# Optimization experiments

Hardware: AMD Instinct MI355X
Metric: run time of the kernel (lower is better)

Reference implementation:

```python
import jax, jax.numpy as jnp
import numpy as np

NUM_ITEMS = 50000
IN_FEATS = 64
H_FEATS = 64
NUM_EDGES = 800000


def setup_inputs() -> dict:
    key = jax.random.key(0)
    ks = jax.random.split(key, 12)
    s_in = 1.0 / np.sqrt(IN_FEATS)
    s_h = 1.0 / np.sqrt(H_FEATS)
    return {
        "embed": jax.random.normal(ks[0], (NUM_ITEMS, IN_FEATS), jnp.float32),
        "W1_self": jax.random.normal(ks[1], (IN_FEATS, H_FEATS), jnp.float32) * s_in,
        "W1_neigh": jax.random.normal(ks[2], (IN_FEATS, H_FEATS), jnp.float32) * s_in,
        "b1": jax.random.normal(ks[3], (H_FEATS,), jnp.float32) * s_in,
        "W2_self": jax.random.normal(ks[4], (H_FEATS, H_FEATS), jnp.float32) * s_h,
        "W2_neigh": jax.random.normal(ks[5], (H_FEATS, H_FEATS), jnp.float32) * s_h,
        "b2": jax.random.normal(ks[6], (H_FEATS,), jnp.float32) * s_h,
        "W_fc": jax.random.normal(ks[7], (H_FEATS, IN_FEATS), jnp.float32) * s_h,
        "b_fc": jax.random.normal(ks[8], (IN_FEATS,), jnp.float32) * s_h,
        "item_ids": jnp.arange(NUM_ITEMS, dtype=jnp.int64),
        "src": jax.random.randint(ks[9], (NUM_EDGES,), 0, NUM_ITEMS, jnp.int64),
        "dst": jax.random.randint(ks[10], (NUM_EDGES,), 0, NUM_ITEMS, jnp.int64),
    }


def _sage_mean(h, src, dst, W_self, W_neigh, b, num_nodes):
    # gather src features along edges, mean-reduce into dst nodes
    agg = jax.ops.segment_sum(h[src], dst, num_segments=num_nodes)  # [N, d]
    deg = jax.ops.segment_sum(jnp.ones_like(dst, dtype=h.dtype), dst,
                              num_segments=num_nodes)
    h_neigh = agg / jnp.clip(deg, 1.0, None)[:, None]  # zero for isolated nodes
    return h @ W_self + h_neigh @ W_neigh + b


def reference(embed, W1_self, W1_neigh, b1, W2_self, W2_neigh, b2,
              W_fc, b_fc, item_ids, src, dst):
    n = embed.shape[0]
    x = embed[item_ids]                                   # embedding lookup [N, in]
    h = _sage_mean(x, src, dst, W1_self, W1_neigh, b1, n)  # SAGEConv 1
    h = jax.nn.relu(h)
    h = _sage_mean(h, src, dst, W2_self, W2_neigh, b2, n)  # SAGEConv 2
    return h @ W_fc + b_fc                                 # final linear
```

## Files before the change

### kernel.cpp

```cpp
#include <hip/hip_runtime.h>

#define NN 50000
#define NE 800000
#define F  64
#define AT 68
#define SCAN_B 49

__device__ __forceinline__ unsigned bf16rne(float f) {
    unsigned u = __float_as_uint(f);
    return (u + 0x7fffu + ((u >> 16) & 1u)) >> 16;
}
__device__ __forceinline__ float bflo(unsigned p) { return __uint_as_float(p << 16); }
__device__ __forceinline__ float bfhi(unsigned p) { return __uint_as_float(p & 0xffff0000u); }


__global__ void k_count_pos(const int* __restrict__ dst, int* __restrict__ cnt,
                            int* __restrict__ pos) {
    int e = blockIdx.x * blockDim.x + threadIdx.x;
    if (e < NE) pos[e] = atomicAdd(&cnt[dst[e]], 1);
}


__launch_bounds__(256)
__global__ void k_scan_a(const int* __restrict__ cnt, int* __restrict__ partials) {
    __shared__ int sc[256];
    int t = threadIdx.x;
    int base = blockIdx.x * 1024 + t * 4;
    int s = 0;
#pragma unroll
    for (int k = 0; k < 4; ++k) {
        int idx = base + k;
        s += (idx < NN) ? cnt[idx] : 0;
    }
    sc[t] = s;
    __syncthreads();
    for (int d = 128; d > 0; d >>= 1) {
        if (t < d) sc[t] += sc[t + d];
        __syncthreads();
    }
    if (t == 0) partials[blockIdx.x] = sc[0];
}

__launch_bounds__(64)
__global__ void k_scan_b(const int* __restrict__ partials, int* __restrict__ blockoff,
                         int* __restrict__ offs_last) {
    int t = threadIdx.x;
    int v = (t < SCAN_B) ? partials[t] : 0;
    int orig = v;
    for (int d = 1; d < 64; d <<= 1) {
        int u = __shfl_up(v, d);
        if (t >= d) v += u;
    }
    if (t < SCAN_B) blockoff[t] = v - orig;
    if (t == 63) *offs_last = v;
}

__launch_bounds__(256)
__global__ void k_scan_c(const int* __restrict__ cnt, const int* __restrict__ blockoff,
                         int* __restrict__ offs) {
    __shared__ int sc[256];
    int t = threadIdx.x;
    int base = blockIdx.x * 1024 + t * 4;
    int v[4];
#pragma unroll
    for (int k = 0; k < 4; ++k) {
        int idx = base + k;
        v[k] = (idx < NN) ? cnt[idx] : 0;
    }
    int lsum = v[0] + v[1] + v[2] + v[3];
    sc[t] = lsum;
    __syncthreads();
    for (int d = 1; d < 256; d <<= 1) {
        int u = (t >= d) ? sc[t - d] : 0;
        __syncthreads();
        sc[t] += u;
        __syncthreads();
    }
    int run = blockoff[blockIdx.x] + sc[t] - lsum;
#pragma unroll
    for (int k = 0; k < 4; ++k) {
        int idx = base + k;
        if (idx < NN) { offs[idx] = run; run += v[k]; }
    }
}

__global__ void k_fill(const int* __restrict__ src, const int* __restrict__ dst,
                       const int* __restrict__ offs, const int* __restrict__ pos,
                       int* __restrict__ csr) {
    int e = blockIdx.x * blockDim.x + threadIdx.x;
    if (e < NE) csr[offs[dst[e]] + pos[e]] = src[e];
}


__global__ void k_gather(const float* __restrict__ embed, const int* __restrict__ ids,
                         uint2* __restrict__ xb) {
    int t = blockIdx.x * blockDim.x + threadIdx.x;
    if (t < NN * 16) {
        int i = t >> 4, c = t & 15;
        float4 v = ((const float4*)embed)[ids[i] * 16 + c];
        uint2 p;
        p.x = bf16rne(v.x) | (bf16rne(v.y) << 16);
        p.y = bf16rne(v.z) | (bf16rne(v.w) << 16);
        xb[t] = p;
    }
}


__device__ __forceinline__ void add8(float s[8], const uint4 v) {
    s[0] += bflo(v.x); s[1] += bfhi(v.x);
    s[2] += bflo(v.y); s[3] += bfhi(v.y);
    s[4] += bflo(v.z); s[5] += bfhi(v.z);
    s[6] += bflo(v.w); s[7] += bfhi(v.w);
}

__launch_bounds__(256)
__global__ void k_aggb(const uint4* __restrict__ inb, const int* __restrict__ offs,
                       const int* __restrict__ csr, uint4* __restrict__ hnb) {
    int g = (blockIdx.x * 256 + threadIdx.x) >> 3;
    int c = threadIdx.x & 7;
    if (g >= NN) return;
    int lane = threadIdx.x & 63;
    int base = lane & 56;
    int beg = offs[g], end = offs[g + 1];
    float s[8] = {0.f, 0.f, 0.f, 0.f, 0.f, 0.f, 0.f, 0.f};
    int j = beg;
    for (; j + 8 <= end; j += 8) {
        int v = csr[j + c];
        int i0 = __shfl(v, base + 0, 64), i1 = __shfl(v, base + 1, 64);
        int i2 = __shfl(v, base + 2, 64), i3 = __shfl(v, base + 3, 64);
        int i4 = __shfl(v, base + 4, 64), i5 = __shfl(v, base + 5, 64);
        int i6 = __shfl(v, base + 6, 64), i7 = __shfl(v, base + 7, 64);
        uint4 d0 = inb[i0 * 8 + c], d1 = inb[i1 * 8 + c];
        uint4 d2 = inb[i2 * 8 + c], d3 = inb[i3 * 8 + c];
        uint4 d4 = inb[i4 * 8 + c], d5 = inb[i5 * 8 + c];
        uint4 d6 = inb[i6 * 8 + c], d7 = inb[i7 * 8 + c];
        add8(s, d0); add8(s, d1); add8(s, d2); add8(s, d3);
        add8(s, d4); add8(s, d5); add8(s, d6); add8(s, d7);
    }
    int rem = end - j;
    if (rem > 0) {
        int v = csr[j + (c < rem ? c : 0)];
        int idx[8];
#pragma unroll
        for (int k = 0; k < 8; ++k) idx[k] = __shfl(v, base + k, 64);
#pragma unroll
        for (int k = 0; k < 8; ++k)
            if (k < rem) { uint4 d = inb[idx[k] * 8 + c]; add8(s, d); }
    }
    int deg = end - beg;
    float inv = (deg > 0) ? 1.f / (float)deg : 0.f;
    uint4 o;
    o.x = bf16rne(s[0] * inv) | (bf16rne(s[1] * inv) << 16);
    o.y = bf16rne(s[2] * inv) | (bf16rne(s[3] * inv) << 16);
    o.z = bf16rne(s[4] * inv) | (bf16rne(s[5] * inv) << 16);
    o.w = bf16rne(s[6] * inv) | (bf16rne(s[7] * inv) << 16);
    hnb[g * 8 + c] = o;
}


template <bool RELU, bool EMITB>
__launch_bounds__(256)
__global__ void k_layer2(const float* __restrict__ X, const int* __restrict__ ids,
                         const uint4* __restrict__ Nhb,
                         const float* __restrict__ Ws, const float* __restrict__ Wn,
                         const float* __restrict__ b, float* __restrict__ out,
                         uint2* __restrict__ outb) {
    __shared__ alignas(16) float AsT[F * AT];
    __shared__ alignas(16) float NsT[F * AT];
    __shared__ alignas(16) float WsL[F * F];
    __shared__ alignas(16) float WnL[F * F];

    const int tid = threadIdx.x;
    const int node0 = blockIdx.x * 64;

    for (int idx = tid; idx < F * F / 4; idx += 256) {
        ((float4*)WsL)[idx] = ((const float4*)Ws)[idx];
        ((float4*)WnL)[idx] = ((const float4*)Wn)[idx];
    }
    for (int idx = tid; idx < 64 * 16; idx += 256) {
        int n = idx >> 4, c = idx & 15;
        int node = node0 + n;
        float4 a = make_float4(0.f, 0.f, 0.f, 0.f);
        if (node < NN) {
            int row = ids ? ids[node] : node;
            a = ((const float4*)X)[row * 16 + c];
        }
        int f = 4 * c;
        AsT[(f + 0) * AT + n] = a.x; AsT[(f + 1) * AT + n] = a.y;
        AsT[(f + 2) * AT + n] = a.z; AsT[(f + 3) * AT + n] = a.w;
    }
    for (int idx = tid; idx < 64 * 8; idx += 256) {
        int n = idx >> 3, c = idx & 7;
        int node = node0 + n;
        uint4 v = make_uint4(0u, 0u, 0u, 0u);
        if (node < NN) v = Nhb[node * 8 + c];
        int f = 8 * c;
        NsT[(f + 0) * AT + n] = bflo(v.x); NsT[(f + 1) * AT + n] = bfhi(v.x);
        NsT[(f + 2) * AT + n] = bflo(v.y); NsT[(f + 3) * AT + n] = bfhi(v.y);
        NsT[(f + 4) * AT + n] = bflo(v.z); NsT[(f + 5) * AT + n] = bfhi(v.z);
        NsT[(f + 6) * AT + n] = bflo(v.w); NsT[(f + 7) * AT + n] = bfhi(v.w);
    }
    __syncthreads();

    const int tx = tid & 15, ty = tid >> 4;
    float acc[4][4];
#pragma unroll
    for (int j = 0; j < 4; ++j) {
        float bv = b[4 * tx + j];
        acc[0][j] = bv; acc[1][j] = bv; acc[2][j] = bv; acc[3][j] = bv;
    }
#pragma unroll 4
    for (int k = 0; k < 64; ++k) {
        float4 a4 = *(const float4*)&AsT[k * AT + 4 * ty];
        float4 n4 = *(const float4*)&NsT[k * AT + 4 * ty];
        float4 w4 = *(const float4*)&WsL[k * 64 + 4 * tx];
        float4 u4 = *(const float4*)&WnL[k * 64 + 4 * tx];
        float a_[4] = {a4.x, a4.y, a4.z, a4.w};
        float n_[4] = {n4.x, n4.y, n4.z, n4.w};
        float w_[4] = {w4.x, w4.y, w4.z, w4.w};
        float u_[4] = {u4.x, u4.y, u4.z, u4.w};
#pragma unroll
        for (int i = 0; i < 4; ++i)
#pragma unroll
            for (int j = 0; j < 4; ++j)
                acc[i][j] += a_[i] * w_[j] + n_[i] * u_[j];
    }

#pragma unroll
    for (int i = 0; i < 4; ++i) {
        int node = node0 + 4 * ty + i;
        if (node < NN) {
            float4 o;
            o.x = acc[i][0]; o.y = acc[i][1]; o.z = acc[i][2]; o.w = acc[i][3];
            if (RELU) {
                o.x = o.x > 0.f ? o.x : 0.f;
                o.y = o.y > 0.f ? o.y : 0.f;
                o.z = o.z > 0.f ? o.z : 0.f;
                o.w = o.w > 0.f ? o.w : 0.f;
            }
            *(float4*)&out[node * 64 + 4 * tx] = o;
            if (EMITB) {
                uint2 p;
                p.x = bf16rne(o.x) | (bf16rne(o.y) << 16);
                p.y = bf16rne(o.z) | (bf16rne(o.w) << 16);
                outb[node * 16 + tx] = p;
            }
        }
    }
}


__launch_bounds__(256)
__global__ void k_final(const float* __restrict__ X, const float* __restrict__ W,
                        const float* __restrict__ b, float* __restrict__ out) {
    __shared__ alignas(16) float AsT[F * AT];
    __shared__ alignas(16) float WL[F * F];

    const int tid = threadIdx.x;
    const int node0 = blockIdx.x * 64;

    for (int idx = tid; idx < F * F / 4; idx += 256)
        ((float4*)WL)[idx] = ((const float4*)W)[idx];
    for (int idx = tid; idx < 64 * 16; idx += 256) {
        int n = idx >> 4, c = idx & 15;
        int node = node0 + n;
        float4 a = make_float4(0.f, 0.f, 0.f, 0.f);
        if (node < NN) a = ((const float4*)X)[node * 16 + c];
        int f = 4 * c;
        AsT[(f + 0) * AT + n] = a.x; AsT[(f + 1) * AT + n] = a.y;
        AsT[(f + 2) * AT + n] = a.z; AsT[(f + 3) * AT + n] = a.w;
    }
    __syncthreads();

    const int tx = tid & 15, ty = tid >> 4;
    float acc[4][4];
#pragma unroll
    for (int j = 0; j < 4; ++j) {
        float bv = b[4 * tx + j];
        acc[0][j] = bv; acc[1][j] = bv; acc[2][j] = bv; acc[3][j] = bv;
    }
#pragma unroll 4
    for (int k = 0; k < 64; ++k) {
        float4 a4 = *(const float4*)&AsT[k * AT + 4 * ty];
        float4 w4 = *(const float4*)&WL[k * 64 + 4 * tx];
        float a_[4] = {a4.x, a4.y, a4.z, a4.w};
        float w_[4] = {w4.x, w4.y, w4.z, w4.w};
#pragma unroll
        for (int i = 0; i < 4; ++i)
#pragma unroll
            for (int j = 0; j < 4; ++j)
                acc[i][j] += a_[i] * w_[j];
    }
#pragma unroll
    for (int i = 0; i < 4; ++i) {
        int node = node0 + 4 * ty + i;
        if (node < NN) {
            float4 o;
            o.x = acc[i][0]; o.y = acc[i][1]; o.z = acc[i][2]; o.w = acc[i][3];
            *(float4*)&out[node * 64 + 4 * tx] = o;
        }
    }
}


extern "C" void kernel_launch(void* const* d_in, const int* in_sizes, int n_in,
                              void* d_out, int out_size, void* d_ws, size_t ws_size,
                              hipStream_t stream) {
    const float* embed = (const float*)d_in[0];
    const float* W1s = (const float*)d_in[1];
    const float* W1n = (const float*)d_in[2];
    const float* b1  = (const float*)d_in[3];
    const float* W2s = (const float*)d_in[4];
    const float* W2n = (const float*)d_in[5];
    const float* b2  = (const float*)d_in[6];
    const float* Wfc = (const float*)d_in[7];
    const float* bfc = (const float*)d_in[8];
    const int* ids = (const int*)d_in[9];
    const int* src = (const int*)d_in[10];
    const int* dst = (const int*)d_in[11];
    float* out = (float*)d_out;

    char* ws = (char*)d_ws;
    size_t off = 0;
    auto alloc = [&](size_t nb) {
        char* p = ws + off;
        off = (off + nb + 255) & ~(size_t)255;
        return p;
    };
    int*   cnt      = (int*)alloc(NN * sizeof(int));
    size_t zero_bytes = off;
    int*   offs     = (int*)alloc((NN + 1) * sizeof(int));
    int*   partials = (int*)alloc(SCAN_B * sizeof(int));
    int*   blockoff = (int*)alloc(SCAN_B * sizeof(int));
    int*   pos      = (int*)alloc(NE * sizeof(int));
    int*   csr      = (int*)alloc(NE * sizeof(int));
    uint2* xb       = (uint2*)alloc((size_t)NN * 16 * sizeof(uint2));
    uint2* h1b      = (uint2*)alloc((size_t)NN * 16 * sizeof(uint2));
    uint4* hnb      = (uint4*)alloc((size_t)NN * 8 * sizeof(uint4));
    float* h1       = (float*)alloc((size_t)NN * F * sizeof(float));
    float* h2       = (float*)alloc((size_t)NN * F * sizeof(float));

    hipMemsetAsync(d_ws, 0, zero_bytes, stream);

    const int TB = 256;
    k_count_pos<<<(NE + TB - 1) / TB, TB, 0, stream>>>(dst, cnt, pos);
    k_scan_a<<<SCAN_B, 256, 0, stream>>>(cnt, partials);
    k_scan_b<<<1, 64, 0, stream>>>(partials, blockoff, &offs[NN]);
    k_scan_c<<<SCAN_B, 256, 0, stream>>>(cnt, blockoff, offs);
    k_fill<<<(NE + TB - 1) / TB, TB, 0, stream>>>(src, dst, offs, pos, csr);
    k_gather<<<(NN * 16 + TB - 1) / TB, TB, 0, stream>>>(embed, ids, xb);

    const int NB = (NN + 63) / 64;
    const int AB = (NN * 8 + 255) / 256;

    k_aggb<<<AB, TB, 0, stream>>>((const uint4*)xb, offs, csr, hnb);
    k_layer2<true, true><<<NB, TB, 0, stream>>>(embed, ids, hnb, W1s, W1n, b1, h1, h1b);
    k_aggb<<<AB, TB, 0, stream>>>((const uint4*)h1b, offs, csr, hnb);
    k_layer2<false, false><<<NB, TB, 0, stream>>>(h1, nullptr, hnb, W2s, W2n, b2, h2, nullptr);
    k_final<<<NB, TB, 0, stream>>>(h2, Wfc, bfc, out);
}
```

Baseline: 243.1 us.

## Fuse count with gather, merge scan stages, and fold final linear into layer two

Merges the degree counting and embedding bf16 gather into one kernel, and folds the single-block scan into the per-block scan so every block recomputes the block offsets. Layer two now reads the bf16 copy of h1 instead of an fp32 h1 and applies the final linear in the same kernel through shared memory, so the fp32 h1 and h2 buffers are never written or read back. This cuts launch count and global traffic. In exchange, layer two's self term now uses bf16-rounded h1, which loses some precision.

```diff
diff --git a/kernel.cpp b/kernel.cpp
--- a/kernel.cpp
+++ b/kernel.cpp
@@ -14,87 +14,13 @@
 __device__ __forceinline__ float bfhi(unsigned p) { return __uint_as_float(p & 0xffff0000u); }
 
 
-__global__ void k_count_pos(const int* __restrict__ dst, int* __restrict__ cnt,
-                            int* __restrict__ pos) {
-    int e = blockIdx.x * blockDim.x + threadIdx.x;
-    if (e < NE) pos[e] = atomicAdd(&cnt[dst[e]], 1);
-}
-
-
-__launch_bounds__(256)
-__global__ void k_scan_a(const int* __restrict__ cnt, int* __restrict__ partials) {
-    __shared__ int sc[256];
-    int t = threadIdx.x;
-    int base = blockIdx.x * 1024 + t * 4;
-    int s = 0;
-#pragma unroll
-    for (int k = 0; k < 4; ++k) {
-        int idx = base + k;
-        s += (idx < NN) ? cnt[idx] : 0;
-    }
-    sc[t] = s;
-    __syncthreads();
-    for (int d = 128; d > 0; d >>= 1) {
-        if (t < d) sc[t] += sc[t + d];
-        __syncthreads();
-    }
-    if (t == 0) partials[blockIdx.x] = sc[0];
-}
-
-__launch_bounds__(64)
-__global__ void k_scan_b(const int* __restrict__ partials, int* __restrict__ blockoff,
-                         int* __restrict__ offs_last) {
-    int t = threadIdx.x;
-    int v = (t < SCAN_B) ? partials[t] : 0;
-    int orig = v;
-    for (int d = 1; d < 64; d <<= 1) {
-        int u = __shfl_up(v, d);
-        if (t >= d) v += u;
-    }
-    if (t < SCAN_B) blockoff[t] = v - orig;
-    if (t == 63) *offs_last = v;
-}
-
-__launch_bounds__(256)
-__global__ void k_scan_c(const int* __restrict__ cnt, const int* __restrict__ blockoff,
-                         int* __restrict__ offs) {
-    __shared__ int sc[256];
-    int t = threadIdx.x;
-    int base = blockIdx.x * 1024 + t * 4;
-    int v[4];
-#pragma unroll
-    for (int k = 0; k < 4; ++k) {
-        int idx = base + k;
-        v[k] = (idx < NN) ? cnt[idx] : 0;
-    }
-    int lsum = v[0] + v[1] + v[2] + v[3];
-    sc[t] = lsum;
-    __syncthreads();
-    for (int d = 1; d < 256; d <<= 1) {
-        int u = (t >= d) ? sc[t - d] : 0;
-        __syncthreads();
-        sc[t] += u;
-        __syncthreads();
-    }
-    int run = blockoff[blockIdx.x] + sc[t] - lsum;
-#pragma unroll
-    for (int k = 0; k < 4; ++k) {
-        int idx = base + k;
-        if (idx < NN) { offs[idx] = run; run += v[k]; }
-    }
-}
-
-__global__ void k_fill(const int* __restrict__ src, const int* __restrict__ dst,
-                       const int* __restrict__ offs, const int* __restrict__ pos,
-                       int* __restrict__ csr) {
-    int e = blockIdx.x * blockDim.x + threadIdx.x;
-    if (e < NE) csr[offs[dst[e]] + pos[e]] = src[e];
-}
-
-
-__global__ void k_gather(const float* __restrict__ embed, const int* __restrict__ ids,
-                         uint2* __restrict__ xb) {
+__launch_bounds__(256)
+__global__ void k_count_gather(const int* __restrict__ dst, int* __restrict__ cnt,
+                               int* __restrict__ pos,
+                               const float* __restrict__ embed, const int* __restrict__ ids,
+                               uint2* __restrict__ xb) {
     int t = blockIdx.x * blockDim.x + threadIdx.x;
+    if (t < NE) pos[t] = atomicAdd(&cnt[dst[t]], 1);
     if (t < NN * 16) {
         int i = t >> 4, c = t & 15;
         float4 v = ((const float4*)embed)[ids[i] * 16 + c];
@@ -103,6 +29,76 @@
         p.y = bf16rne(v.z) | (bf16rne(v.w) << 16);
         xb[t] = p;
     }
+}
+
+
+__launch_bounds__(256)
+__global__ void k_scan_a(const int* __restrict__ cnt, int* __restrict__ partials) {
+    __shared__ int sc[256];
+    int t = threadIdx.x;
+    int base = blockIdx.x * 1024 + t * 4;
+    int s = 0;
+#pragma unroll
+    for (int k = 0; k < 4; ++k) {
+        int idx = base + k;
+        s += (idx < NN) ? cnt[idx] : 0;
+    }
+    sc[t] = s;
+    __syncthreads();
+    for (int d = 128; d > 0; d >>= 1) {
+        if (t < d) sc[t] += sc[t + d];
+        __syncthreads();
+    }
+    if (t == 0) partials[blockIdx.x] = sc[0];
+}
+
+__launch_bounds__(256)
+__global__ void k_scan_c2(const int* __restrict__ cnt, const int* __restrict__ partials,
+                          int* __restrict__ offs) {
+    __shared__ int sboff;
+    __shared__ int stotal;
+    __shared__ int sc[256];
+    int t = threadIdx.x;
+    if (t < 64) {
+        int v = (t < SCAN_B) ? partials[t] : 0;
+        int orig = v;
+        for (int d = 1; d < 64; d <<= 1) {
+            int u = __shfl_up(v, d);
+            if (t >= d) v += u;
+        }
+        if (t == (int)blockIdx.x) sboff = v - orig;
+        if (t == 63) stotal = v;
+    }
+    int base = blockIdx.x * 1024 + t * 4;
+    int v4[4];
+#pragma unroll
+    for (int k = 0; k < 4; ++k) {
+        int idx = base + k;
+        v4[k] = (idx < NN) ? cnt[idx] : 0;
+    }
+    int lsum = v4[0] + v4[1] + v4[2] + v4[3];
+    sc[t] = lsum;
+    __syncthreads();
+    for (int d = 1; d < 256; d <<= 1) {
+        int u = (t >= d) ? sc[t - d] : 0;
+        __syncthreads();
+        sc[t] += u;
+        __syncthreads();
+    }
+    int run = sboff + sc[t] - lsum;
+#pragma unroll
+    for (int k = 0; k < 4; ++k) {
+        int idx = base + k;
+        if (idx < NN) { offs[idx] = run; run += v4[k]; }
+    }
+    if (blockIdx.x == 0 && t == 0) offs[NN] = stotal;
+}
+
+__global__ void k_fill(const int* __restrict__ src, const int* __restrict__ dst,
+                       const int* __restrict__ offs, const int* __restrict__ pos,
+                       int* __restrict__ csr) {
+    int e = blockIdx.x * blockDim.x + threadIdx.x;
+    if (e < NE) csr[offs[dst[e]] + pos[e]] = src[e];
 }
 
 
@@ -158,13 +154,11 @@
 }
 
 
-template <bool RELU, bool EMITB>
-__launch_bounds__(256)
-__global__ void k_layer2(const float* __restrict__ X, const int* __restrict__ ids,
-                         const uint4* __restrict__ Nhb,
-                         const float* __restrict__ Ws, const float* __restrict__ Wn,
-                         const float* __restrict__ b, float* __restrict__ out,
-                         uint2* __restrict__ outb) {
+__launch_bounds__(256)
+__global__ void k_layer_mid(const float* __restrict__ X, const int* __restrict__ ids,
+                            const uint4* __restrict__ Nhb,
+                            const float* __restrict__ Ws, const float* __restrict__ Wn,
+                            const float* __restrict__ b, uint2* __restrict__ outb) {
     __shared__ alignas(16) float AsT[F * AT];
     __shared__ alignas(16) float NsT[F * AT];
     __shared__ alignas(16) float WsL[F * F];
@@ -181,10 +175,7 @@
         int n = idx >> 4, c = idx & 15;
         int node = node0 + n;
         float4 a = make_float4(0.f, 0.f, 0.f, 0.f);
-        if (node < NN) {
-            int row = ids ? ids[node] : node;
-            a = ((const float4*)X)[row * 16 + c];
-        }
+        if (node < NN) a = ((const float4*)X)[ids[node] * 16 + c];
         int f = 4 * c;
         AsT[(f + 0) * AT + n] = a.x; AsT[(f + 1) * AT + n] = a.y;
         AsT[(f + 2) * AT + n] = a.z; AsT[(f + 3) * AT + n] = a.w;
@@ -230,45 +221,58 @@
     for (int i = 0; i < 4; ++i) {
         int node = node0 + 4 * ty + i;
         if (node < NN) {
-            float4 o;
-            o.x = acc[i][0]; o.y = acc[i][1]; o.z = acc[i][2]; o.w = acc[i][3];
-            if (RELU) {
-                o.x = o.x > 0.f ? o.x : 0.f;
-                o.y = o.y > 0.f ? o.y : 0.f;
-                o.z = o.z > 0.f ? o.z : 0.f;
-                o.w = o.w > 0.f ? o.w : 0.f;
-            }
-            *(float4*)&out[node * 64 + 4 * tx] = o;
-            if (EMITB) {
-                uint2 p;
-                p.x = bf16rne(o.x) | (bf16rne(o.y) << 16);
-                p.y = bf16rne(o.z) | (bf16rne(o.w) << 16);
-                outb[node * 16 + tx] = p;
-            }
+            float ox = acc[i][0] > 0.f ? acc[i][0] : 0.f;
+            float oy = acc[i][1] > 0.f ? acc[i][1] : 0.f;
+            float oz = acc[i][2] > 0.f ? acc[i][2] : 0.f;
+            float ow = acc[i][3] > 0.f ? acc[i][3] : 0.f;
+            uint2 p;
+            p.x = bf16rne(ox) | (bf16rne(oy) << 16);
+            p.y = bf16rne(oz) | (bf16rne(ow) << 16);
+            outb[node * 16 + tx] = p;
         }
     }
 }
 
 
 __launch_bounds__(256)
-__global__ void k_final(const float* __restrict__ X, const float* __restrict__ W,
-                        const float* __restrict__ b, float* __restrict__ out) {
+__global__ void k_layer_last(const uint4* __restrict__ Ab, const uint4* __restrict__ Nhb,
+                             const float* __restrict__ Ws, const float* __restrict__ Wn,
+                             const float* __restrict__ b,
+                             const float* __restrict__ Wfc, const float* __restrict__ bfc,
+                             float* __restrict__ out) {
     __shared__ alignas(16) float AsT[F * AT];
-    __shared__ alignas(16) float WL[F * F];
+    __shared__ alignas(16) float NsT[F * AT];
+    __shared__ alignas(16) float WsL[F * F];
+    __shared__ alignas(16) float WnL[F * F];
 
     const int tid = threadIdx.x;
     const int node0 = blockIdx.x * 64;
 
-    for (int idx = tid; idx < F * F / 4; idx += 256)
-        ((float4*)WL)[idx] = ((const float4*)W)[idx];
-    for (int idx = tid; idx < 64 * 16; idx += 256) {
-        int n = idx >> 4, c = idx & 15;
+    for (int idx = tid; idx < F * F / 4; idx += 256) {
+        ((float4*)WsL)[idx] = ((const float4*)Ws)[idx];
+        ((float4*)WnL)[idx] = ((const float4*)Wn)[idx];
+    }
+    for (int idx = tid; idx < 64 * 8; idx += 256) {
+        int n = idx >> 3, c = idx & 7;
         int node = node0 + n;
-        float4 a = make_float4(0.f, 0.f, 0.f, 0.f);
-        if (node < NN) a = ((const float4*)X)[node * 16 + c];
-        int f = 4 * c;
-        AsT[(f + 0) * AT + n] = a.x; AsT[(f + 1) * AT + n] = a.y;
-        AsT[(f + 2) * AT + n] = a.z; AsT[(f + 3) * AT + n] = a.w;
+        uint4 v = make_uint4(0u, 0u, 0u, 0u);
+        if (node < NN) v = Ab[node * 8 + c];
+        int f = 8 * c;
+        AsT[(f + 0) * AT + n] = bflo(v.x); AsT[(f + 1) * AT + n] = bfhi(v.x);
+        AsT[(f + 2) * AT + n] = bflo(v.y); AsT[(f + 3) * AT + n] = bfhi(v.y);
+        AsT[(f + 4) * AT + n] = bflo(v.z); AsT[(f + 5) * AT + n] = bfhi(v.z);
+        AsT[(f + 6) * AT + n] = bflo(v.w); AsT[(f + 7) * AT + n] = bfhi(v.w);
+    }
+    for (int idx = tid; idx < 64 * 8; idx += 256) {
+        int n = idx >> 3, c = idx & 7;
+        int node = node0 + n;
+        uint4 v = make_uint4(0u, 0u, 0u, 0u);
+        if (node < NN) v = Nhb[node * 8 + c];
+        int f = 8 * c;
+        NsT[(f + 0) * AT + n] = bflo(v.x); NsT[(f + 1) * AT + n] = bfhi(v.x);
+        NsT[(f + 2) * AT + n] = bflo(v.y); NsT[(f + 3) * AT + n] = bfhi(v.y);
+        NsT[(f + 4) * AT + n] = bflo(v.z); NsT[(f + 5) * AT + n] = bfhi(v.z);
+        NsT[(f + 6) * AT + n] = bflo(v.w); NsT[(f + 7) * AT + n] = bfhi(v.w);
     }
     __syncthreads();
 
@@ -282,21 +286,54 @@
 #pragma unroll 4
     for (int k = 0; k < 64; ++k) {
         float4 a4 = *(const float4*)&AsT[k * AT + 4 * ty];
-        float4 w4 = *(const float4*)&WL[k * 64 + 4 * tx];
+        float4 n4 = *(const float4*)&NsT[k * AT + 4 * ty];
+        float4 w4 = *(const float4*)&WsL[k * 64 + 4 * tx];
+        float4 u4 = *(const float4*)&WnL[k * 64 + 4 * tx];
+        float a_[4] = {a4.x, a4.y, a4.z, a4.w};
+        float n_[4] = {n4.x, n4.y, n4.z, n4.w};
+        float w_[4] = {w4.x, w4.y, w4.z, w4.w};
+        float u_[4] = {u4.x, u4.y, u4.z, u4.w};
+#pragma unroll
+        for (int i = 0; i < 4; ++i)
+#pragma unroll
+            for (int j = 0; j < 4; ++j)
+                acc[i][j] += a_[i] * w_[j] + n_[i] * u_[j];
+    }
+
+    __syncthreads();
+#pragma unroll
+    for (int i = 0; i < 4; ++i)
+#pragma unroll
+        for (int j = 0; j < 4; ++j)
+            AsT[(4 * tx + j) * AT + (4 * ty + i)] = acc[i][j];
+    for (int idx = tid; idx < F * F / 4; idx += 256)
+        ((float4*)WsL)[idx] = ((const float4*)Wfc)[idx];
+    __syncthreads();
+
+    float acc2[4][4];
+#pragma unroll
+    for (int j = 0; j < 4; ++j) {
+        float bv = bfc[4 * tx + j];
+        acc2[0][j] = bv; acc2[1][j] = bv; acc2[2][j] = bv; acc2[3][j] = bv;
+    }
+#pragma unroll 4
+    for (int k = 0; k < 64; ++k) {
+        float4 a4 = *(const float4*)&AsT[k * AT + 4 * ty];
+        float4 w4 = *(const float4*)&WsL[k * 64 + 4 * tx];
         float a_[4] = {a4.x, a4.y, a4.z, a4.w};
         float w_[4] = {w4.x, w4.y, w4.z, w4.w};
 #pragma unroll
         for (int i = 0; i < 4; ++i)
 #pragma unroll
             for (int j = 0; j < 4; ++j)
-                acc[i][j] += a_[i] * w_[j];
+                acc2[i][j] += a_[i] * w_[j];
     }
 #pragma unroll
     for (int i = 0; i < 4; ++i) {
         int node = node0 + 4 * ty + i;
         if (node < NN) {
             float4 o;
-            o.x = acc[i][0]; o.y = acc[i][1]; o.z = acc[i][2]; o.w = acc[i][3];
+            o.x = acc2[i][0]; o.y = acc2[i][1]; o.z = acc2[i][2]; o.w = acc2[i][3];
             *(float4*)&out[node * 64 + 4 * tx] = o;
         }
     }
@@ -331,31 +368,26 @@
     size_t zero_bytes = off;
     int*   offs     = (int*)alloc((NN + 1) * sizeof(int));
     int*   partials = (int*)alloc(SCAN_B * sizeof(int));
-    int*   blockoff = (int*)alloc(SCAN_B * sizeof(int));
     int*   pos      = (int*)alloc(NE * sizeof(int));
     int*   csr      = (int*)alloc(NE * sizeof(int));
     uint2* xb       = (uint2*)alloc((size_t)NN * 16 * sizeof(uint2));
     uint2* h1b      = (uint2*)alloc((size_t)NN * 16 * sizeof(uint2));
     uint4* hnb      = (uint4*)alloc((size_t)NN * 8 * sizeof(uint4));
-    float* h1       = (float*)alloc((size_t)NN * F * sizeof(float));
-    float* h2       = (float*)alloc((size_t)NN * F * sizeof(float));
 
     hipMemsetAsync(d_ws, 0, zero_bytes, stream);
 
     const int TB = 256;
-    k_count_pos<<<(NE + TB - 1) / TB, TB, 0, stream>>>(dst, cnt, pos);
+    const int EB = (NE + TB - 1) / TB;
+    k_count_gather<<<EB, TB, 0, stream>>>(dst, cnt, pos, embed, ids, xb);
     k_scan_a<<<SCAN_B, 256, 0, stream>>>(cnt, partials);
-    k_scan_b<<<1, 64, 0, stream>>>(partials, blockoff, &offs[NN]);
-    k_scan_c<<<SCAN_B, 256, 0, stream>>>(cnt, blockoff, offs);
-    k_fill<<<(NE + TB - 1) / TB, TB, 0, stream>>>(src, dst, offs, pos, csr);
-    k_gather<<<(NN * 16 + TB - 1) / TB, TB, 0, stream>>>(embed, ids, xb);
+    k_scan_c2<<<SCAN_B, 256, 0, stream>>>(cnt, partials, offs);
+    k_fill<<<EB, TB, 0, stream>>>(src, dst, offs, pos, csr);
 
     const int NB = (NN + 63) / 64;
     const int AB = (NN * 8 + 255) / 256;
 
     k_aggb<<<AB, TB, 0, stream>>>((const uint4*)xb, offs, csr, hnb);
-    k_layer2<true, true><<<NB, TB, 0, stream>>>(embed, ids, hnb, W1s, W1n, b1, h1, h1b);
+    k_layer_mid<<<NB, TB, 0, stream>>>(embed, ids, hnb, W1s, W1n, b1, h1b);
     k_aggb<<<AB, TB, 0, stream>>>((const uint4*)h1b, offs, csr, hnb);
-    k_layer2<false, false><<<NB, TB, 0, stream>>>(h1, nullptr, hnb, W2s, W2n, b2, h2, nullptr);
-    k_final<<<NB, TB, 0, stream>>>(h2, Wfc, bfc, out);
-}
+    k_layer_last<<<NB, TB, 0, stream>>>((const uint4*)h1b, hnb, W2s, W2n, b2, Wfc, bfc, out);
+}
```

New measurement: 236.0 us. 1.03x faster.
